# Performance work log

Hardware: AMD Instinct MI355X
Metric: run time of the kernel (lower is better)

Reference implementation:

```python
import jax, jax.numpy as jnp
import numpy as np

N_POINTS = 32
N_HEADS = 4
EMBED = 256
TAU = 2.0


def _grid_sample_bilinear(val, gx, gy):
    # val: [N, C, H, W]; gx, gy: [N, Q, P] normalized coords in [-1, 1]
    # bilinear, padding_mode='zeros', align_corners=False
    N, C, H, W = val.shape
    ix = (gx + 1.0) * (W * 0.5) - 0.5
    iy = (gy + 1.0) * (H * 0.5) - 0.5
    x0 = jnp.floor(ix)
    y0 = jnp.floor(iy)
    x1 = x0 + 1.0
    y1 = y0 + 1.0
    wx1 = ix - x0
    wx0 = 1.0 - wx1
    wy1 = iy - y0
    wy0 = 1.0 - wy1
    gather = jax.vmap(lambda v, yy, xx: v[:, yy, xx])  # per-image advanced-index gather
    out = jnp.zeros((N, C) + gx.shape[1:], dtype=val.dtype)
    for xs, ys, wx, wy in ((x0, y0, wx0, wy0), (x1, y0, wx1, wy0),
                           (x0, y1, wx0, wy1), (x1, y1, wx1, wy1)):
        m = ((xs >= 0) & (xs < W) & (ys >= 0) & (ys < H)).astype(val.dtype) * wx * wy
        xi = jnp.clip(xs, 0, W - 1).astype(jnp.int32)
        yi = jnp.clip(ys, 0, H - 1).astype(jnp.int32)
        out = out + gather(val, yi, xi) * m[:, None]
    return out  # [N, C, Q, P]


def setup_inputs() -> dict:
    key = jax.random.key(0)
    ks = jax.random.split(key, 18)
    B, L = 2, 1000
    lvl_hw = [(256, 256), (128, 128), (64, 64), (32, 32)]
    inp = {}
    for i, (h, w) in enumerate(lvl_hw):
        inp[f'value{i}'] = jax.random.normal(ks[i], (B, EMBED, h, w), jnp.float32)
    inp['query_content'] = jax.random.normal(ks[4], (B, L, EMBED), jnp.float32)
    img = 1024.0
    xy = jax.random.uniform(ks[5], (B, L, 2), minval=0.0, maxval=img)
    z = jax.random.uniform(ks[6], (B, L, 1), minval=4.0, maxval=6.5)
    r = jax.random.uniform(ks[7], (B, L, 1), minval=-0.8, maxval=0.8)
    th = jax.random.uniform(ks[8], (B, L, 1), minval=-np.pi, maxval=np.pi)
    inp['query_xyzrt'] = jnp.concatenate([xy, z, r, th], axis=-1).astype(jnp.float32)
    inp['strides'] = jnp.array([4, 8, 16, 32], jnp.int32)
    s = 0.02
    inp['W_off'] = jax.random.normal(ks[9], (EMBED, N_HEADS * N_POINTS * 3)) * s
    inp['b_off'] = jax.random.normal(ks[10], (N_HEADS * N_POINTS * 3,)) * 0.2
    inp['W_ca1'] = jax.random.normal(ks[11], (EMBED, EMBED // 4)) * s
    inp['W_ca2'] = jax.random.normal(ks[12], (EMBED // 4, EMBED)) * s
    inp['W_sa1'] = jax.random.normal(ks[13], (EMBED, EMBED // 4)) * s
    inp['W_sa2'] = jax.random.normal(ks[14], (EMBED // 4, N_HEADS * N_POINTS)) * s
    inp['W_out'] = jax.random.normal(ks[15], (EMBED * N_POINTS, EMBED)) * s
    inp['b_out'] = jnp.zeros((EMBED,), jnp.float32)
    return inp


def reference(value0, value1, value2, value3, query_content, query_xyzrt, strides,
              W_off, b_off, W_ca1, W_ca2, W_sa1, W_sa2, W_out, b_out):
    values = [value0, value1, value2, value3]
    B, L, _ = query_content.shape
    P = N_HEADS * N_POINTS
    G = N_HEADS
    ch = EMBED // G

    # ---- make_sample_points ----
    offset = (query_content @ W_off + b_off).reshape(B, L, P, 3)
    roi_cc = query_xyzrt[..., :2]                      # [B,L,2]
    scale = 2.0 ** query_xyzrt[..., 2:3]
    ratio = 2.0 ** jnp.concatenate([query_xyzrt[..., 3:4] * -0.5,
                                    query_xyzrt[..., 3:4] * 0.5], axis=-1)
    roi_wh = scale * ratio                             # [B,L,2]
    theta = query_xyzrt[..., 4]
    c, s = jnp.cos(theta), jnp.sin(theta)
    R = jnp.stack([jnp.stack([c, -s], -1), jnp.stack([s, c], -1)], -2)  # [B,L,2,2]
    off_xy = offset[..., :2] * roi_wh[:, :, None, :]
    rot_xy = jnp.einsum('blpj,blij->blpi', off_xy, R)  # offset @ R^T
    sample_xy = roi_cc[:, :, None, :] + rot_xy         # [B,L,P,2] absolute coords
    sample_z = query_xyzrt[..., 2][:, :, None] + offset[..., 2]  # [B,L,P]

    # ---- level weights: sigmoid(-(z - log2(stride))^2 / tau) ----
    grid = jnp.log2(strides.astype(sample_z.dtype))    # [n_levels]
    lvl_w = jax.nn.sigmoid(-((sample_z[..., None] - grid) ** 2) / TAU)  # [B,L,P,n_lvl]

    # ---- multi-level rotated deformable sampling ----
    sampling_value = jnp.zeros((B, L, G, N_POINTS, ch), query_content.dtype)
    for lvl, v in enumerate(values):
        H, W = v.shape[2], v.shape[3]
        stride_f = strides[lvl].astype(sample_xy.dtype)
        mapping = jnp.stack([W * stride_f, H * stride_f])  # (x_extent, y_extent)
        norm_xy = sample_xy / mapping * 2.0 - 1.0          # [B,L,P,2] in [-1,1]
        # split points into head groups: [B,L,G,pts,2] -> [B*G, L, pts, 2]
        g_xy = norm_xy.reshape(B, L, G, N_POINTS, 2).transpose(0, 2, 1, 3, 4).reshape(B * G, L, N_POINTS, 2)
        v_g = v.reshape(B * G, ch, H, W)
        out = _grid_sample_bilinear(v_g, g_xy[..., 0], g_xy[..., 1])  # [B*G, ch, L, pts]
        w = lvl_w[..., lvl].reshape(B, L, G, N_POINTS).transpose(0, 2, 1, 3).reshape(B * G, 1, L, N_POINTS)
        out = out * w
        sampling_value = sampling_value + out.reshape(B, G, ch, L, N_POINTS).transpose(0, 3, 1, 4, 2)

    # ---- channel / spatial attention gates ----
    ca = jax.nn.sigmoid(jax.nn.relu(query_content @ W_ca1) @ W_ca2)
    ca = ca.reshape(B, L, G, 1, ch)
    sa = jax.nn.sigmoid(jax.nn.relu(query_content @ W_sa1) @ W_sa2)
    sa = sa.reshape(B, L, G, N_POINTS, 1)
    out = sampling_value * ca * sa
    out = out.reshape(B, L, G * N_POINTS * ch) @ W_out + b_out
    return out + query_content
```

## Files before the change

### kernel.cpp

```cpp
#include <hip/hip_runtime.h>

#define NQ    2000
#define KDIM  8192
#define EMB   256
#define MPAD  2048
#define SPLITK 8

typedef __attribute__((ext_vector_type(8))) short bf16x8;
typedef __attribute__((ext_vector_type(4))) float f32x4;

__device__ __forceinline__ float sigf(float x) { return 1.0f / (1.0f + __expf(-x)); }

__device__ __forceinline__ unsigned short f2bf(float x) {
    union { float f; unsigned int u; } v; v.f = x;
    unsigned int r = v.u + 0x7fffu + ((v.u >> 16) & 1u);
    return (unsigned short)(r >> 16);
}

__global__ __launch_bounds__(256) void prep_kernel(
    const float* __restrict__ qc, const float* __restrict__ xyzrt,
    const float* __restrict__ Woff, const float* __restrict__ boff,
    const float* __restrict__ Wca1, const float* __restrict__ Wca2,
    const float* __restrict__ Wsa1, const float* __restrict__ Wsa2,
    float* __restrict__ qdata)
{
    const int q = blockIdx.x;
    const int t = threadIdx.x;
    __shared__ float qs[256];
    __shared__ float offs[384];
    __shared__ float h1[64];
    __shared__ float h2[64];
    __shared__ float sas[128];

    qs[t] = qc[(size_t)q * 256 + t];
    __syncthreads();

    for (int item = t; item < 512; item += 256) {
        float acc = 0.f;
        if (item < 384) {
            const float* w = Woff + item;
            #pragma unroll 8
            for (int k = 0; k < 256; k++) acc = fmaf(qs[k], w[(size_t)k * 384], acc);
            offs[item] = acc + boff[item];
        } else if (item < 448) {
            const int j = item - 384;
            const float* w = Wca1 + j;
            #pragma unroll 8
            for (int k = 0; k < 256; k++) acc = fmaf(qs[k], w[(size_t)k * 64], acc);
            h1[j] = fmaxf(acc, 0.f);
        } else {
            const int j = item - 448;
            const float* w = Wsa1 + j;
            #pragma unroll 8
            for (int k = 0; k < 256; k++) acc = fmaf(qs[k], w[(size_t)k * 64], acc);
            h2[j] = fmaxf(acc, 0.f);
        }
    }
    __syncthreads();

    {
        float acc = 0.f;
        #pragma unroll 8
        for (int j = 0; j < 64; j++) acc = fmaf(h1[j], Wca2[(size_t)j * 256 + t], acc);
        float* qd = qdata + (size_t)q * 1024;
        qd[768 + t] = sigf(acc);
        if (t < 128) {
            float a2 = 0.f;
            #pragma unroll 8
            for (int j = 0; j < 64; j++) a2 = fmaf(h2[j], Wsa2[(size_t)j * 128 + t], a2);
            sas[t] = sigf(a2);
        }
    }
    __syncthreads();

    if (t < 128) {
        const int p = t;
        float* qd = qdata + (size_t)q * 1024;
        const float x  = xyzrt[(size_t)q * 5 + 0];
        const float y  = xyzrt[(size_t)q * 5 + 1];
        const float z  = xyzrt[(size_t)q * 5 + 2];
        const float r  = xyzrt[(size_t)q * 5 + 3];
        const float th = xyzrt[(size_t)q * 5 + 4];
        const float sc  = exp2f(z);
        const float rw  = sc * exp2f(-0.5f * r);
        const float rh  = sc * exp2f( 0.5f * r);
        const float cth = __cosf(th), sth = __sinf(th);
        const float ox = offs[p * 3 + 0] * rw;
        const float oy = offs[p * 3 + 1] * rh;
        qd[p]       = x + cth * ox - sth * oy;
        qd[128 + p] = y + sth * ox + cth * oy;
        const float sz = z + offs[p * 3 + 2];
        const float sa = sas[p];
        #pragma unroll
        for (int l = 0; l < 4; l++) {
            const float d = sz - (float)(2 + l);
            qd[256 + p * 4 + l] = sigf(-0.5f * d * d) * sa;
        }
    }
}

__global__ __launch_bounds__(256) void transpose_kernel(
    const float* __restrict__ v, unsigned short* __restrict__ vt, int H)
{
    int bid = blockIdx.x;
    const int y  = bid % H;            bid /= H;
    const int xt = bid % (H >> 5);     bid /= (H >> 5);
    const int ct = bid & 3;
    const int b  = bid >> 2;
    const int t  = threadIdx.x;

    __shared__ float tile[64][33];
    const float* src = v + ((size_t)(b * 256 + ct * 64) * H + y) * H + xt * 32;
    const int xi = t & 31;
    #pragma unroll
    for (int i = 0; i < 8; i++) {
        const int c = (t >> 5) + i * 8;
        tile[c][xi] = src[(size_t)c * H * H + xi];
    }
    __syncthreads();
    unsigned short* dst = vt + (((size_t)(b * H + y) * H + xt * 32) * 256) + ct * 64;
    const int ci = (t & 31) * 2;
    #pragma unroll
    for (int i = 0; i < 4; i++) {
        const int x2 = (t >> 5) + i * 8;
        ushort2 pk;
        pk.x = f2bf(tile[ci][x2]);
        pk.y = f2bf(tile[ci + 1][x2]);
        *(ushort2*)(dst + (size_t)x2 * 256 + ci) = pk;
    }
}

__global__ __launch_bounds__(256) void wconvert_kernel(
    const float* __restrict__ W, unsigned short* __restrict__ Wt)
{
    const int kt = blockIdx.x & 255;
    const int nt = blockIdx.x >> 8;
    const int k0 = kt * 32, n0 = nt * 32;
    const int t = threadIdx.x;
    __shared__ float tile[32][33];
    #pragma unroll
    for (int i = 0; i < 4; i++) {
        const int ki = (t >> 5) + i * 8;
        tile[ki][t & 31] = W[(size_t)(k0 + ki) * 256 + n0 + (t & 31)];
    }
    __syncthreads();
    #pragma unroll
    for (int i = 0; i < 4; i++) {
        const int ni = (t >> 5) + i * 8;
        const int ki = t & 31;
        Wt[(size_t)(n0 + ni) * KDIM + k0 + ki] = f2bf(tile[ki][ni]);
    }
}

__global__ __launch_bounds__(256) void sample_kernel(
    const unsigned short* __restrict__ v0, const unsigned short* __restrict__ v1,
    const unsigned short* __restrict__ v2, const unsigned short* __restrict__ v3,
    const float* __restrict__ qdata,
    unsigned short* __restrict__ X)
{
    const int wid  = blockIdx.x * 4 + (threadIdx.x >> 6);
    const int lane = threadIdx.x & 63;
    const int q  = wid >> 4;
    const int pb = (wid & 15) * 8;
    const int pt = lane >> 3;
    const int gp = pb + pt;
    const int g  = gp >> 5;
    const int c8 = (lane & 7) * 8;
    const int b  = (q >= 1000) ? 1 : 0;

    const float* qd = qdata + (size_t)q * 1024;
    const float px = qd[gp];
    const float py = qd[128 + gp];
    float wlv[4];
    #pragma unroll
    for (int l = 0; l < 4; l++) wlv[l] = qd[256 + gp * 4 + l];

    const unsigned short* vals[4] = { v0, v1, v2, v3 };
    const int cbase = g * 64 + c8;

    float acc[8] = {};
    #pragma unroll
    for (int l = 0; l < 4; l++) {
        const int   H   = 256 >> l;
        const float inv = 1.0f / (float)(4 << l);
        const float wl  = wlv[l];
        const float ix = px * inv - 0.5f;
        const float iy = py * inv - 0.5f;
        const float x0f = floorf(ix), y0f = floorf(iy);
        const int   x0 = (int)x0f,    y0 = (int)y0f;
        const float fx1 = ix - x0f, fx0 = 1.f - fx1;
        const float fy1 = iy - y0f, fy0 = 1.f - fy1;
        const bool xi0 = (x0 >= 0) & (x0 < H);
        const bool xi1 = (x0 + 1 >= 0) & (x0 + 1 < H);
        const bool yi0 = (y0 >= 0) & (y0 < H);
        const bool yi1 = (y0 + 1 >= 0) & (y0 + 1 < H);
        const int xc0 = min(max(x0, 0), H - 1);
        const int xc1 = min(max(x0 + 1, 0), H - 1);
        const int yc0 = min(max(y0, 0), H - 1);
        const int yc1 = min(max(y0 + 1, 0), H - 1);
        const float m00 = (xi0 & yi0) ? wl * fx0 * fy0 : 0.f;
        const float m10 = (xi1 & yi0) ? wl * fx1 * fy0 : 0.f;
        const float m01 = (xi0 & yi1) ? wl * fx0 * fy1 : 0.f;
        const float m11 = (xi1 & yi1) ? wl * fx1 * fy1 : 0.f;

        const unsigned short* base = vals[l] + (size_t)b * H * H * 256 + cbase;
        const int ry0 = yc0 * H, ry1 = yc1 * H;
        const uint4 d00 = *(const uint4*)(base + (size_t)(ry0 + xc0) * 256);
        const uint4 d10 = *(const uint4*)(base + (size_t)(ry0 + xc1) * 256);
        const uint4 d01 = *(const uint4*)(base + (size_t)(ry1 + xc0) * 256);
        const uint4 d11 = *(const uint4*)(base + (size_t)(ry1 + xc1) * 256);

        const uint4 dv[4] = { d00, d10, d01, d11 };
        const float mv[4] = { m00, m10, m01, m11 };
        #pragma unroll
        for (int tap = 0; tap < 4; tap++) {
            const unsigned int du[4] = { dv[tap].x, dv[tap].y, dv[tap].z, dv[tap].w };
            const float m = mv[tap];
            #pragma unroll
            for (int i = 0; i < 4; i++) {
                union { unsigned int u; float f; } lo, hi;
                lo.u = du[i] << 16;
                hi.u = du[i] & 0xffff0000u;
                acc[2 * i]     = fmaf(m, lo.f, acc[2 * i]);
                acc[2 * i + 1] = fmaf(m, hi.f, acc[2 * i + 1]);
            }
        }
    }

    const float* caf = qd + 768 + cbase;
    const float4 ca0 = *(const float4*)caf;
    const float4 ca1 = *(const float4*)(caf + 4);
    const float cav[8] = { ca0.x, ca0.y, ca0.z, ca0.w, ca1.x, ca1.y, ca1.z, ca1.w };
    uint4 o;
    unsigned int* op = (unsigned int*)&o;
    #pragma unroll
    for (int i = 0; i < 4; i++) {
        const unsigned int lo = f2bf(acc[2 * i] * cav[2 * i]);
        const unsigned int hi = f2bf(acc[2 * i + 1] * cav[2 * i + 1]);
        op[i] = lo | (hi << 16);
    }
    *(uint4*)(X + (size_t)q * KDIM + pb * 64 + lane * 8) = o;
}

#define LSTR 56

__global__ __launch_bounds__(256) void gemm_kernel(
    const unsigned short* __restrict__ X,
    const unsigned short* __restrict__ Wt,
    float* __restrict__ part)
{
    __shared__ unsigned short Xs[64][LSTR];
    __shared__ unsigned short Ws[64][LSTR];
    const int m0 = blockIdx.x * 64;
    const int n0 = blockIdx.y * 64;
    const int z  = blockIdx.z;
    const int t  = threadIdx.x;
    const int w    = t >> 6;
    const int lane = t & 63;
    const int mw = (w & 1) * 32;
    const int nw = (w >> 1) * 32;
    const int quad = lane >> 4;
    const int l16  = lane & 15;

    const int srow = t >> 2;
    const int koff = (t & 3) * 8;

    f32x4 acc[2][2] = {};

    const int kbase = z * (KDIM / SPLITK);
    for (int kt = 0; kt < KDIM / SPLITK; kt += 32) {
        const int k0 = kbase + kt;
        {
            const int m = m0 + srow;
            uint4 xv = make_uint4(0, 0, 0, 0);
            if (m < NQ) xv = *(const uint4*)(X + (size_t)m * KDIM + k0 + koff);
            *(uint4*)&Xs[srow][koff] = xv;
            *(uint4*)&Ws[srow][koff] = *(const uint4*)(Wt + (size_t)(n0 + srow) * KDIM + k0 + koff);
        }
        __syncthreads();
        bf16x8 a0 = *(const bf16x8*)&Xs[mw + l16     ][quad * 8];
        bf16x8 a1 = *(const bf16x8*)&Xs[mw + l16 + 16][quad * 8];
        bf16x8 b0 = *(const bf16x8*)&Ws[nw + l16     ][quad * 8];
        bf16x8 b1 = *(const bf16x8*)&Ws[nw + l16 + 16][quad * 8];
        acc[0][0] = __builtin_amdgcn_mfma_f32_16x16x32_bf16(a0, b0, acc[0][0], 0, 0, 0);
        acc[0][1] = __builtin_amdgcn_mfma_f32_16x16x32_bf16(a0, b1, acc[0][1], 0, 0, 0);
        acc[1][0] = __builtin_amdgcn_mfma_f32_16x16x32_bf16(a1, b0, acc[1][0], 0, 0, 0);
        acc[1][1] = __builtin_amdgcn_mfma_f32_16x16x32_bf16(a1, b1, acc[1][1], 0, 0, 0);
        __syncthreads();
    }

    float* pz = part + (size_t)z * MPAD * EMB;
    #pragma unroll
    for (int i = 0; i < 2; i++) {
        #pragma unroll
        for (int j = 0; j < 2; j++) {
            const int n = n0 + nw + 16 * j + l16;
            #pragma unroll
            for (int r = 0; r < 4; r++) {
                const int m = m0 + mw + 16 * i + quad * 4 + r;
                pz[(size_t)m * EMB + n] = acc[i][j][r];
            }
        }
    }
}

__global__ __launch_bounds__(256) void reduce_kernel(
    const float* __restrict__ part, const float* __restrict__ qc,
    const float* __restrict__ bias, float* __restrict__ out)
{
    const int idx = blockIdx.x * 256 + threadIdx.x;
    if (idx >= NQ * 64) return;
    const int m  = idx >> 6;
    const int c4 = idx & 63;
    float4 a = ((const float4*)bias)[c4];
    const float4 qv = ((const float4*)qc)[(size_t)m * 64 + c4];
    a.x += qv.x; a.y += qv.y; a.z += qv.z; a.w += qv.w;
    #pragma unroll
    for (int z = 0; z < SPLITK; z++) {
        const float4 p = ((const float4*)part)[((size_t)z * MPAD + m) * 64 + c4];
        a.x += p.x; a.y += p.y; a.z += p.z; a.w += p.w;
    }
    ((float4*)out)[(size_t)m * 64 + c4] = a;
}

extern "C" void kernel_launch(void* const* d_in, const int* in_sizes, int n_in,
                              void* d_out, int out_size, void* d_ws, size_t ws_size,
                              hipStream_t stream) {
    (void)in_sizes; (void)n_in; (void)out_size; (void)ws_size;
    const float* v0    = (const float*)d_in[0];
    const float* v1    = (const float*)d_in[1];
    const float* v2    = (const float*)d_in[2];
    const float* v3    = (const float*)d_in[3];
    const float* qc    = (const float*)d_in[4];
    const float* xyzrt = (const float*)d_in[5];
    const float* Woff  = (const float*)d_in[7];
    const float* boff  = (const float*)d_in[8];
    const float* Wca1  = (const float*)d_in[9];
    const float* Wca2  = (const float*)d_in[10];
    const float* Wsa1  = (const float*)d_in[11];
    const float* Wsa2  = (const float*)d_in[12];
    const float* Wout  = (const float*)d_in[13];
    const float* bout  = (const float*)d_in[14];
    float* out = (float*)d_out;

    char* p = (char*)d_ws;
    float* qdata = (float*)p;                 p += (size_t)NQ * 1024 * 4;
    unsigned short* Xb = (unsigned short*)p;  p += (size_t)NQ * KDIM * 2;
    unsigned short* vt0 = (unsigned short*)p; p += (size_t)2 * 256 * 256 * 256 * 2;
    unsigned short* vt1 = (unsigned short*)p; p += (size_t)2 * 128 * 128 * 256 * 2;
    unsigned short* vt2 = (unsigned short*)p; p += (size_t)2 * 64 * 64 * 256 * 2;
    unsigned short* vt3 = (unsigned short*)p; p += (size_t)2 * 32 * 32 * 256 * 2;
    unsigned short* Wtb = (unsigned short*)p; p += (size_t)EMB * KDIM * 2;
    float* partb = (float*)p;

    prep_kernel<<<NQ, 256, 0, stream>>>(qc, xyzrt, Woff, boff, Wca1, Wca2, Wsa1, Wsa2, qdata);
    transpose_kernel<<<2 * 4 * (256 / 32) * 256, 256, 0, stream>>>(v0, vt0, 256);
    transpose_kernel<<<2 * 4 * (128 / 32) * 128, 256, 0, stream>>>(v1, vt1, 128);
    transpose_kernel<<<2 * 4 * (64 / 32) * 64,   256, 0, stream>>>(v2, vt2, 64);
    transpose_kernel<<<2 * 4 * (32 / 32) * 32,   256, 0, stream>>>(v3, vt3, 32);
    wconvert_kernel<<<2048, 256, 0, stream>>>(Wout, Wtb);
    sample_kernel<<<(NQ * 128) / (4 * 8), 256, 0, stream>>>(vt0, vt1, vt2, vt3, qdata, Xb);
    gemm_kernel<<<dim3(MPAD / 64, EMB / 64, SPLITK), 256, 0, stream>>>(Xb, Wtb, partb);
    reduce_kernel<<<(NQ * 64 + 255) / 256, 256, 0, stream>>>(partb, qc, bout, out);
}
```

Measured before the change: 391.9 us.

## Move query projections to split-bf16 MFMA GEMM, fuse prep launches, drop LDS in GEMM

The per-query scalar projection kernel becomes three stages. The first converts the query and projection weights to hi/lo bf16 pairs inside one merged conversion kernel that also does the value transposes and the Wout conversion. The second is a 3-pass bf16 MFMA GEMM that approximates fp32 accuracy. The third is a batched finish kernel handling 8 queries per block for the gates and the sampling geometry. The output GEMM now loads operands directly from global memory into registers instead of staging them through LDS with barriers. The intent is to cut scalar FMA work and launch count, at the cost of extra workspace and slightly different numerics. The X buffer grows to MPAD rows, but the sampler does not fill the padding rows, so the GEMM reads uninitialized data for rows that are later discarded.

```diff
diff --git a/kernel.cpp b/kernel.cpp
--- a/kernel.cpp
+++ b/kernel.cpp
@@ -16,139 +16,210 @@
     unsigned int r = v.u + 0x7fffu + ((v.u >> 16) & 1u);
     return (unsigned short)(r >> 16);
 }
-
-__global__ __launch_bounds__(256) void prep_kernel(
-    const float* __restrict__ qc, const float* __restrict__ xyzrt,
-    const float* __restrict__ Woff, const float* __restrict__ boff,
-    const float* __restrict__ Wca1, const float* __restrict__ Wca2,
-    const float* __restrict__ Wsa1, const float* __restrict__ Wsa2,
+__device__ __forceinline__ float bf2f(unsigned short h) {
+    union { unsigned int u; float f; } v; v.u = ((unsigned int)h) << 16; return v.f;
+}
+
+__global__ __launch_bounds__(256) void trans_kernel(
+    const float* __restrict__ v0, const float* __restrict__ v1,
+    const float* __restrict__ v2, const float* __restrict__ v3,
+    unsigned short* __restrict__ vt0, unsigned short* __restrict__ vt1,
+    unsigned short* __restrict__ vt2, unsigned short* __restrict__ vt3,
+    const float* __restrict__ Wout, unsigned short* __restrict__ Wtb,
+    const float* __restrict__ Woff, const float* __restrict__ Wca1,
+    const float* __restrict__ Wsa1,
+    unsigned short* __restrict__ WH, unsigned short* __restrict__ WL,
+    const float* __restrict__ qc,
+    unsigned short* __restrict__ qcH, unsigned short* __restrict__ qcL)
+{
+    __shared__ float tile[64][33];
+    int bid = blockIdx.x;
+    const int t = threadIdx.x;
+
+    if (bid < 21760) {
+        const float* v; unsigned short* vt; int H;
+        if (bid < 16384)      { v = v0; vt = vt0; H = 256; }
+        else if (bid < 20480) { bid -= 16384; v = v1; vt = vt1; H = 128; }
+        else if (bid < 21504) { bid -= 20480; v = v2; vt = vt2; H = 64; }
+        else                  { bid -= 21504; v = v3; vt = vt3; H = 32; }
+        const int y  = bid % H;            bid /= H;
+        const int xt = bid % (H >> 5);     bid /= (H >> 5);
+        const int ct = bid & 3;
+        const int b  = bid >> 2;
+        const float* src = v + ((size_t)(b * 256 + ct * 64) * H + y) * H + xt * 32;
+        const int xi = t & 31;
+        #pragma unroll
+        for (int i = 0; i < 8; i++) {
+            const int c = (t >> 5) + i * 8;
+            tile[c][xi] = src[(size_t)c * H * H + xi];
+        }
+        __syncthreads();
+        unsigned short* dst = vt + (((size_t)(b * H + y) * H + xt * 32) * 256) + ct * 64;
+        const int ci = (t & 31) * 2;
+        #pragma unroll
+        for (int i = 0; i < 4; i++) {
+            const int x2 = (t >> 5) + i * 8;
+            ushort2 pk;
+            pk.x = f2bf(tile[ci][x2]);
+            pk.y = f2bf(tile[ci + 1][x2]);
+            *(ushort2*)(dst + (size_t)x2 * 256 + ci) = pk;
+        }
+    } else if (bid < 23808) {
+        const int local = bid - 21760;
+        const int k0 = (local & 255) * 32, n0 = (local >> 8) * 32;
+        float (*tl)[33] = tile;
+        #pragma unroll
+        for (int i = 0; i < 4; i++) {
+            const int ki = (t >> 5) + i * 8;
+            tl[ki][t & 31] = Wout[(size_t)(k0 + ki) * 256 + n0 + (t & 31)];
+        }
+        __syncthreads();
+        #pragma unroll
+        for (int i = 0; i < 4; i++) {
+            const int ni = (t >> 5) + i * 8;
+            const int ki = t & 31;
+            Wtb[(size_t)(n0 + ni) * KDIM + k0 + ki] = f2bf(tl[ki][ni]);
+        }
+    } else if (bid < 24320) {
+        const int n = bid - 23808;
+        float val;
+        if (n < 384)      val = Woff[(size_t)t * 384 + n];
+        else if (n < 448) val = Wca1[(size_t)t * 64 + (n - 384)];
+        else              val = Wsa1[(size_t)t * 64 + (n - 448)];
+        const unsigned short hh = f2bf(val);
+        WH[(size_t)n * 256 + t] = hh;
+        WL[(size_t)n * 256 + t] = f2bf(val - bf2f(hh));
+    } else {
+        const int q = bid - 24320;
+        const float val = (q < NQ) ? qc[(size_t)q * 256 + t] : 0.f;
+        const unsigned short hh = f2bf(val);
+        qcH[(size_t)q * 256 + t] = hh;
+        qcL[(size_t)q * 256 + t] = f2bf(val - bf2f(hh));
+    }
+}
+
+__global__ __launch_bounds__(256) void gemmA_kernel(
+    const unsigned short* __restrict__ qcH, const unsigned short* __restrict__ qcL,
+    const unsigned short* __restrict__ WH,  const unsigned short* __restrict__ WL,
+    float* __restrict__ Hout)
+{
+    const int m0 = blockIdx.x * 64;
+    const int n0 = blockIdx.y * 64;
+    const int t  = threadIdx.x;
+    const int w    = t >> 6;
+    const int lane = t & 63;
+    const int mw = (w & 1) * 32;
+    const int nw = (w >> 1) * 32;
+    const int quad = lane >> 4;
+    const int l16  = lane & 15;
+
+    f32x4 acc[2][2] = {};
+    #pragma unroll
+    for (int pass = 0; pass < 3; pass++) {
+        const unsigned short* Ap = (pass == 2) ? qcL : qcH;
+        const unsigned short* Bp = (pass == 1) ? WL : WH;
+        const unsigned short* ar0 = Ap + (size_t)(m0 + mw + l16) * 256 + quad * 8;
+        const unsigned short* ar1 = ar0 + 16 * 256;
+        const unsigned short* br0 = Bp + (size_t)(n0 + nw + l16) * 256 + quad * 8;
+        const unsigned short* br1 = br0 + 16 * 256;
+        #pragma unroll
+        for (int k = 0; k < 256; k += 32) {
+            const bf16x8 a0 = *(const bf16x8*)(ar0 + k);
+            const bf16x8 a1 = *(const bf16x8*)(ar1 + k);
+            const bf16x8 b0 = *(const bf16x8*)(br0 + k);
+            const bf16x8 b1 = *(const bf16x8*)(br1 + k);
+            acc[0][0] = __builtin_amdgcn_mfma_f32_16x16x32_bf16(a0, b0, acc[0][0], 0, 0, 0);
+            acc[0][1] = __builtin_amdgcn_mfma_f32_16x16x32_bf16(a0, b1, acc[0][1], 0, 0, 0);
+            acc[1][0] = __builtin_amdgcn_mfma_f32_16x16x32_bf16(a1, b0, acc[1][0], 0, 0, 0);
+            acc[1][1] = __builtin_amdgcn_mfma_f32_16x16x32_bf16(a1, b1, acc[1][1], 0, 0, 0);
+        }
+    }
+    #pragma unroll
+    for (int i = 0; i < 2; i++)
+        #pragma unroll
+        for (int j = 0; j < 2; j++) {
+            const int n = n0 + nw + 16 * j + l16;
+            #pragma unroll
+            for (int r = 0; r < 4; r++) {
+                const int m = m0 + mw + 16 * i + quad * 4 + r;
+                Hout[(size_t)m * 512 + n] = acc[i][j][r];
+            }
+        }
+}
+
+__global__ __launch_bounds__(256) void finish_kernel(
+    const float* __restrict__ Hbuf, const float* __restrict__ xyzrt,
+    const float* __restrict__ boff,
+    const float* __restrict__ Wca2, const float* __restrict__ Wsa2,
     float* __restrict__ qdata)
 {
-    const int q = blockIdx.x;
-    const int t = threadIdx.x;
-    __shared__ float qs[256];
-    __shared__ float offs[384];
-    __shared__ float h1[64];
-    __shared__ float h2[64];
-    __shared__ float sas[128];
-
-    qs[t] = qc[(size_t)q * 256 + t];
+    const int q0 = blockIdx.x * 8;
+    const int t  = threadIdx.x;
+    __shared__ float hca[8][64];
+    __shared__ float hsa[8][64];
+    __shared__ float sas[8][128];
+
+    for (int i = t; i < 1024; i += 256) {
+        const int q = i >> 7, j = i & 127;
+        const float v = fmaxf(Hbuf[(size_t)(q0 + q) * 512 + 384 + j], 0.f);
+        if (j < 64) hca[q][j] = v; else hsa[q][j - 64] = v;
+    }
     __syncthreads();
 
-    for (int item = t; item < 512; item += 256) {
-        float acc = 0.f;
-        if (item < 384) {
-            const float* w = Woff + item;
-            #pragma unroll 8
-            for (int k = 0; k < 256; k++) acc = fmaf(qs[k], w[(size_t)k * 384], acc);
-            offs[item] = acc + boff[item];
-        } else if (item < 448) {
-            const int j = item - 384;
-            const float* w = Wca1 + j;
-            #pragma unroll 8
-            for (int k = 0; k < 256; k++) acc = fmaf(qs[k], w[(size_t)k * 64], acc);
-            h1[j] = fmaxf(acc, 0.f);
-        } else {
-            const int j = item - 448;
-            const float* w = Wsa1 + j;
-            #pragma unroll 8
-            for (int k = 0; k < 256; k++) acc = fmaf(qs[k], w[(size_t)k * 64], acc);
-            h2[j] = fmaxf(acc, 0.f);
-        }
+    {
+        float acc[8] = {};
+        for (int j = 0; j < 64; j++) {
+            const float wv = Wca2[(size_t)j * 256 + t];
+            #pragma unroll
+            for (int q = 0; q < 8; q++) acc[q] = fmaf(hca[q][j], wv, acc[q]);
+        }
+        #pragma unroll
+        for (int q = 0; q < 8; q++)
+            qdata[(size_t)(q0 + q) * 1024 + 768 + t] = sigf(acc[q]);
+    }
+    {
+        const int c  = t & 127;
+        const int qb = (t >> 7) * 4;
+        float acc[4] = {};
+        for (int j = 0; j < 64; j++) {
+            const float wv = Wsa2[(size_t)j * 128 + c];
+            #pragma unroll
+            for (int qq = 0; qq < 4; qq++) acc[qq] = fmaf(hsa[qb + qq][j], wv, acc[qq]);
+        }
+        #pragma unroll
+        for (int qq = 0; qq < 4; qq++) sas[qb + qq][c] = sigf(acc[qq]);
     }
     __syncthreads();
 
     {
-        float acc = 0.f;
-        #pragma unroll 8
-        for (int j = 0; j < 64; j++) acc = fmaf(h1[j], Wca2[(size_t)j * 256 + t], acc);
-        float* qd = qdata + (size_t)q * 1024;
-        qd[768 + t] = sigf(acc);
-        if (t < 128) {
-            float a2 = 0.f;
-            #pragma unroll 8
-            for (int j = 0; j < 64; j++) a2 = fmaf(h2[j], Wsa2[(size_t)j * 128 + t], a2);
-            sas[t] = sigf(a2);
-        }
-    }
-    __syncthreads();
-
-    if (t < 128) {
-        const int p = t;
-        float* qd = qdata + (size_t)q * 1024;
-        const float x  = xyzrt[(size_t)q * 5 + 0];
-        const float y  = xyzrt[(size_t)q * 5 + 1];
-        const float z  = xyzrt[(size_t)q * 5 + 2];
-        const float r  = xyzrt[(size_t)q * 5 + 3];
-        const float th = xyzrt[(size_t)q * 5 + 4];
-        const float sc  = exp2f(z);
-        const float rw  = sc * exp2f(-0.5f * r);
-        const float rh  = sc * exp2f( 0.5f * r);
-        const float cth = __cosf(th), sth = __sinf(th);
-        const float ox = offs[p * 3 + 0] * rw;
-        const float oy = offs[p * 3 + 1] * rh;
-        qd[p]       = x + cth * ox - sth * oy;
-        qd[128 + p] = y + sth * ox + cth * oy;
-        const float sz = z + offs[p * 3 + 2];
-        const float sa = sas[p];
-        #pragma unroll
-        for (int l = 0; l < 4; l++) {
-            const float d = sz - (float)(2 + l);
-            qd[256 + p * 4 + l] = sigf(-0.5f * d * d) * sa;
-        }
-    }
-}
-
-__global__ __launch_bounds__(256) void transpose_kernel(
-    const float* __restrict__ v, unsigned short* __restrict__ vt, int H)
-{
-    int bid = blockIdx.x;
-    const int y  = bid % H;            bid /= H;
-    const int xt = bid % (H >> 5);     bid /= (H >> 5);
-    const int ct = bid & 3;
-    const int b  = bid >> 2;
-    const int t  = threadIdx.x;
-
-    __shared__ float tile[64][33];
-    const float* src = v + ((size_t)(b * 256 + ct * 64) * H + y) * H + xt * 32;
-    const int xi = t & 31;
-    #pragma unroll
-    for (int i = 0; i < 8; i++) {
-        const int c = (t >> 5) + i * 8;
-        tile[c][xi] = src[(size_t)c * H * H + xi];
-    }
-    __syncthreads();
-    unsigned short* dst = vt + (((size_t)(b * H + y) * H + xt * 32) * 256) + ct * 64;
-    const int ci = (t & 31) * 2;
-    #pragma unroll
-    for (int i = 0; i < 4; i++) {
-        const int x2 = (t >> 5) + i * 8;
-        ushort2 pk;
-        pk.x = f2bf(tile[ci][x2]);
-        pk.y = f2bf(tile[ci + 1][x2]);
-        *(ushort2*)(dst + (size_t)x2 * 256 + ci) = pk;
-    }
-}
-
-__global__ __launch_bounds__(256) void wconvert_kernel(
-    const float* __restrict__ W, unsigned short* __restrict__ Wt)
-{
-    const int kt = blockIdx.x & 255;
-    const int nt = blockIdx.x >> 8;
-    const int k0 = kt * 32, n0 = nt * 32;
-    const int t = threadIdx.x;
-    __shared__ float tile[32][33];
-    #pragma unroll
-    for (int i = 0; i < 4; i++) {
-        const int ki = (t >> 5) + i * 8;
-        tile[ki][t & 31] = W[(size_t)(k0 + ki) * 256 + n0 + (t & 31)];
-    }
-    __syncthreads();
-    #pragma unroll
-    for (int i = 0; i < 4; i++) {
-        const int ni = (t >> 5) + i * 8;
-        const int ki = t & 31;
-        Wt[(size_t)(n0 + ni) * KDIM + k0 + ki] = f2bf(tile[ki][ni]);
+        const int p  = t & 127;
+        const int qb = (t >> 7) * 4;
+        #pragma unroll
+        for (int qq = 0; qq < 4; qq++) {
+            const int q = qb + qq;
+            const float* hrow = Hbuf + (size_t)(q0 + q) * 512 + p * 3;
+            const float o0 = hrow[0] + boff[p * 3 + 0];
+            const float o1 = hrow[1] + boff[p * 3 + 1];
+            const float o2 = hrow[2] + boff[p * 3 + 2];
+            const float* xr = xyzrt + (size_t)(q0 + q) * 5;
+            const float x = xr[0], y = xr[1], z = xr[2], r = xr[3], th = xr[4];
+            const float sc  = exp2f(z);
+            const float rw  = sc * exp2f(-0.5f * r);
+            const float rh  = sc * exp2f( 0.5f * r);
+            const float cth = __cosf(th), sth = __sinf(th);
+            const float ox = o0 * rw;
+            const float oy = o1 * rh;
+            float* qd = qdata + (size_t)(q0 + q) * 1024;
+            qd[p]       = x + cth * ox - sth * oy;
+            qd[128 + p] = y + sth * ox + cth * oy;
+            const float sz = z + o2;
+            const float sa = sas[q][p];
+            #pragma unroll
+            for (int l = 0; l < 4; l++) {
+                const float d = sz - (float)(2 + l);
+                qd[256 + p * 4 + l] = sigf(-0.5f * d * d) * sa;
+            }
+        }
     }
 }
 
@@ -242,15 +313,11 @@
     *(uint4*)(X + (size_t)q * KDIM + pb * 64 + lane * 8) = o;
 }
 
-#define LSTR 56
-
 __global__ __launch_bounds__(256) void gemm_kernel(
     const unsigned short* __restrict__ X,
     const unsigned short* __restrict__ Wt,
     float* __restrict__ part)
 {
-    __shared__ unsigned short Xs[64][LSTR];
-    __shared__ unsigned short Ws[64][LSTR];
     const int m0 = blockIdx.x * 64;
     const int n0 = blockIdx.y * 64;
     const int z  = blockIdx.z;
@@ -262,36 +329,28 @@
     const int quad = lane >> 4;
     const int l16  = lane & 15;
 
-    const int srow = t >> 2;
-    const int koff = (t & 3) * 8;
+    const unsigned short* ar0 = X  + (size_t)(m0 + mw + l16) * KDIM + quad * 8;
+    const unsigned short* ar1 = ar0 + (size_t)16 * KDIM;
+    const unsigned short* br0 = Wt + (size_t)(n0 + nw + l16) * KDIM + quad * 8;
+    const unsigned short* br1 = br0 + (size_t)16 * KDIM;
 
     f32x4 acc[2][2] = {};
-
     const int kbase = z * (KDIM / SPLITK);
-    for (int kt = 0; kt < KDIM / SPLITK; kt += 32) {
-        const int k0 = kbase + kt;
-        {
-            const int m = m0 + srow;
-            uint4 xv = make_uint4(0, 0, 0, 0);
-            if (m < NQ) xv = *(const uint4*)(X + (size_t)m * KDIM + k0 + koff);
-            *(uint4*)&Xs[srow][koff] = xv;
-            *(uint4*)&Ws[srow][koff] = *(const uint4*)(Wt + (size_t)(n0 + srow) * KDIM + k0 + koff);
-        }
-        __syncthreads();
-        bf16x8 a0 = *(const bf16x8*)&Xs[mw + l16     ][quad * 8];
-        bf16x8 a1 = *(const bf16x8*)&Xs[mw + l16 + 16][quad * 8];
-        bf16x8 b0 = *(const bf16x8*)&Ws[nw + l16     ][quad * 8];
-        bf16x8 b1 = *(const bf16x8*)&Ws[nw + l16 + 16][quad * 8];
+    #pragma unroll 4
+    for (int k = kbase; k < kbase + KDIM / SPLITK; k += 32) {
+        const bf16x8 a0 = *(const bf16x8*)(ar0 + k);
+        const bf16x8 a1 = *(const bf16x8*)(ar1 + k);
+        const bf16x8 b0 = *(const bf16x8*)(br0 + k);
+        const bf16x8 b1 = *(const bf16x8*)(br1 + k);
         acc[0][0] = __builtin_amdgcn_mfma_f32_16x16x32_bf16(a0, b0, acc[0][0], 0, 0, 0);
         acc[0][1] = __builtin_amdgcn_mfma_f32_16x16x32_bf16(a0, b1, acc[0][1], 0, 0, 0);
         acc[1][0] = __builtin_amdgcn_mfma_f32_16x16x32_bf16(a1, b0, acc[1][0], 0, 0, 0);
         acc[1][1] = __builtin_amdgcn_mfma_f32_16x16x32_bf16(a1, b1, acc[1][1], 0, 0, 0);
-        __syncthreads();
     }
 
     float* pz = part + (size_t)z * MPAD * EMB;
     #pragma unroll
-    for (int i = 0; i < 2; i++) {
+    for (int i = 0; i < 2; i++)
         #pragma unroll
         for (int j = 0; j < 2; j++) {
             const int n = n0 + nw + 16 * j + l16;
@@ -301,7 +360,6 @@
                 pz[(size_t)m * EMB + n] = acc[i][j][r];
             }
         }
-    }
 }
 
 __global__ __launch_bounds__(256) void reduce_kernel(
@@ -345,20 +403,24 @@
 
     char* p = (char*)d_ws;
     float* qdata = (float*)p;                 p += (size_t)NQ * 1024 * 4;
-    unsigned short* Xb = (unsigned short*)p;  p += (size_t)NQ * KDIM * 2;
+    unsigned short* Xb = (unsigned short*)p;  p += (size_t)MPAD * KDIM * 2;
     unsigned short* vt0 = (unsigned short*)p; p += (size_t)2 * 256 * 256 * 256 * 2;
     unsigned short* vt1 = (unsigned short*)p; p += (size_t)2 * 128 * 128 * 256 * 2;
     unsigned short* vt2 = (unsigned short*)p; p += (size_t)2 * 64 * 64 * 256 * 2;
     unsigned short* vt3 = (unsigned short*)p; p += (size_t)2 * 32 * 32 * 256 * 2;
     unsigned short* Wtb = (unsigned short*)p; p += (size_t)EMB * KDIM * 2;
-    float* partb = (float*)p;
-
-    prep_kernel<<<NQ, 256, 0, stream>>>(qc, xyzrt, Woff, boff, Wca1, Wca2, Wsa1, Wsa2, qdata);
-    transpose_kernel<<<2 * 4 * (256 / 32) * 256, 256, 0, stream>>>(v0, vt0, 256);
-    transpose_kernel<<<2 * 4 * (128 / 32) * 128, 256, 0, stream>>>(v1, vt1, 128);
-    transpose_kernel<<<2 * 4 * (64 / 32) * 64,   256, 0, stream>>>(v2, vt2, 64);
-    transpose_kernel<<<2 * 4 * (32 / 32) * 32,   256, 0, stream>>>(v3, vt3, 32);
-    wconvert_kernel<<<2048, 256, 0, stream>>>(Wout, Wtb);
+    float* partb = (float*)p;                 p += (size_t)SPLITK * MPAD * EMB * 4;
+    float* Hbuf = (float*)p;                  p += (size_t)MPAD * 512 * 4;
+    unsigned short* qcH = (unsigned short*)p; p += (size_t)MPAD * 256 * 2;
+    unsigned short* qcL = (unsigned short*)p; p += (size_t)MPAD * 256 * 2;
+    unsigned short* WHb = (unsigned short*)p; p += (size_t)512 * 256 * 2;
+    unsigned short* WLb = (unsigned short*)p;
+
+    trans_kernel<<<26368, 256, 0, stream>>>(v0, v1, v2, v3, vt0, vt1, vt2, vt3,
+                                            Wout, Wtb, Woff, Wca1, Wsa1,
+                                            WHb, WLb, qc, qcH, qcL);
+    gemmA_kernel<<<dim3(MPAD / 64, 8), 256, 0, stream>>>(qcH, qcL, WHb, WLb, Hbuf);
+    finish_kernel<<<NQ / 8, 256, 0, stream>>>(Hbuf, xyzrt, boff, Wca2, Wsa2, qdata);
     sample_kernel<<<(NQ * 128) / (4 * 8), 256, 0, stream>>>(vt0, vt1, vt2, vt3, qdata, Xb);
     gemm_kernel<<<dim3(MPAD / 64, EMB / 64, SPLITK), 256, 0, stream>>>(Xb, Wtb, partb);
     reduce_kernel<<<(NQ * 64 + 255) / 256, 256, 0, stream>>>(partb, qc, bout, out);
```

Measured after the change: 388.8 us. No clear change (-0.8%).
